# Kernel tuning notes

Measured on AMD Instinct MI355X. Metric: run time of the kernel, lower is better.

Reference implementation:

```python
import jax, jax.numpy as jnp
import numpy as np

DIM = 192
HEADS = 6
WS = 7
N = WS * WS
BW = 4096  # B_ = batch * num_windows
HIDDEN = int(DIM * 4.0)


def _relative_position_index():
    coords = np.stack(np.meshgrid(np.arange(WS), np.arange(WS), indexing='ij'))  # (2,ws,ws)
    cf = coords.reshape(2, -1)                      # (2, N)
    rel = cf[:, :, None] - cf[:, None, :]           # (2, N, N)
    rel = rel.transpose(1, 2, 0)                    # (N, N, 2)
    rel[:, :, 0] += WS - 1
    rel[:, :, 1] += WS - 1
    rel[:, :, 0] *= 2 * WS - 1
    return jnp.asarray(rel.sum(-1), dtype=jnp.int32)  # (N, N)


def setup_inputs() -> dict:
    key = jax.random.key(0)
    ks = jax.random.split(key, 8)
    s = 0.02
    return {
        'x': jax.random.normal(ks[0], (BW, N, DIM), dtype=jnp.float32),
        'ln1_g': jnp.ones((DIM,), jnp.float32),
        'ln1_b': jnp.zeros((DIM,), jnp.float32),
        'qkv_w': jax.random.normal(ks[1], (DIM, 3 * DIM), jnp.float32) * s,  # (in, out)
        'proj_w': jax.random.normal(ks[2], (DIM, DIM), jnp.float32) * s,
        'proj_b': jnp.zeros((DIM,), jnp.float32),
        'bias_table': jax.random.normal(ks[3], ((2 * WS - 1) ** 2, HEADS), jnp.float32) * s,
        'ln2_g': jnp.ones((DIM,), jnp.float32),
        'ln2_b': jnp.zeros((DIM,), jnp.float32),
        'fc1_w': jax.random.normal(ks[4], (DIM, HIDDEN), jnp.float32) * s,
        'fc1_b': jnp.zeros((HIDDEN,), jnp.float32),
        'fc2_w': jax.random.normal(ks[5], (HIDDEN, DIM), jnp.float32) * s,
        'fc2_b': jnp.zeros((DIM,), jnp.float32),
        'rel_index': _relative_position_index(),
    }


def _layer_norm(x, g, b, eps=1e-5):
    mu = jnp.mean(x, axis=-1, keepdims=True)
    var = jnp.var(x, axis=-1, keepdims=True)
    return (x - mu) * jax.lax.rsqrt(var + eps) * g + b


def _window_attention(x, qkv_w, proj_w, proj_b, bias_table, rel_index):
    B_, n, C = x.shape
    hd = C // HEADS
    scale = hd ** -0.5
    qkv = (x @ qkv_w).reshape(B_, n, 3, HEADS, hd)
    q, k, v = (qkv[:, :, i].transpose(0, 2, 1, 3) for i in range(3))  # (B_, h, n, hd)
    attn = jnp.einsum('bhnd,bhmd->bhnm', q * scale, k)
    bias = bias_table[rel_index.reshape(-1)].reshape(n, n, HEADS).transpose(2, 0, 1)
    attn = jax.nn.softmax(attn + bias[None], axis=-1)
    out = jnp.einsum('bhnm,bhmd->bhnd', attn, v).transpose(0, 2, 1, 3).reshape(B_, n, C)
    return out @ proj_w + proj_b


def reference(x, ln1_g, ln1_b, qkv_w, proj_w, proj_b, bias_table,
              ln2_g, ln2_b, fc1_w, fc1_b, fc2_w, fc2_b, rel_index):
    x = x + _window_attention(_layer_norm(x, ln1_g, ln1_b), qkv_w, proj_w, proj_b,
                              bias_table, rel_index)
    h = _layer_norm(x, ln2_g, ln2_b)
    h = jax.nn.gelu(h @ fc1_w + fc1_b, approximate=False) @ fc2_w + fc2_b
    return x + h
```

## Files before the change

### kernel.cpp

```cpp
#include <hip/hip_runtime.h>
#include <cmath>

#define TOK   49
#define WDIM  192
#define NHEADS 6
#define HID   768

typedef __bf16 bf16_t;
typedef bf16_t bf16x8 __attribute__((ext_vector_type(8)));
typedef float  f32x4  __attribute__((ext_vector_type(4)));

#define XLD  200
#define QKLD 72
#define VTLD 72
#define AOLD 72
#define PLD  40
#define HLD2 200

__device__ __forceinline__ f32x4 mfma16(bf16x8 a, bf16x8 b, f32x4 c) {
    return __builtin_amdgcn_mfma_f32_16x16x32_bf16(a, b, c, 0, 0, 0);
}

__device__ __forceinline__ float gelu_f(float v) {
    float u = 0.7978845608028654f * (v + 0.044715f * v * v * v);
    float e = __expf(2.f * u);
    float t = 1.f - 2.f / (e + 1.f);
    return 0.5f * v * (1.f + t);
}

__global__ void pack_w(const float* __restrict__ W, bf16_t* __restrict__ out,
                       int K, int N, int total) {
    int p = blockIdx.x * 256 + threadIdx.x;
    if (p >= total) return;
    int j    = p & 7;
    int lane = (p >> 3) & 63;
    int kbnt = p >> 9;
    int KB   = K >> 5;
    int kb   = kbnt % KB;
    int nt   = kbnt / KB;
    int n = nt * 16 + (lane & 15);
    int k = kb * 32 + (lane >> 4) * 8 + j;
    out[p] = (bf16_t)W[k * N + n];
}

__global__ void make_bias6(const float* __restrict__ table, const int* __restrict__ rel,
                           float* __restrict__ out) {
    int p = blockIdx.x * 256 + threadIdx.x;
    if (p >= NHEADS * TOK * TOK) return;
    int h  = p / (TOK * TOK);
    int mn = p % (TOK * TOK);
    out[p] = table[rel[mn] * NHEADS + h];
}

__global__ void __launch_bounds__(256, 2) attn_kernel(
    const float* __restrict__ x,
    const float* __restrict__ g1, const float* __restrict__ b1,
    const bf16_t* __restrict__ qkv_p, const bf16_t* __restrict__ proj_p,
    const float* __restrict__ proj_b, const float* __restrict__ bias6,
    float* __restrict__ out) {

    __shared__ bf16_t s_xln[64 * XLD];
    __shared__ bf16_t s_q[64 * QKLD];
    __shared__ bf16_t s_k[64 * QKLD];
    __shared__ bf16_t s_vT[64 * VTLD];
    __shared__ bf16_t s_ao[64 * AOLD];
    __shared__ bf16_t s_p[4][16 * PLD];

    const int t    = threadIdx.x;
    const int w    = t >> 6;
    const int lane = t & 63;
    const int l15  = lane & 15;
    const int quad = lane >> 4;
    const int widx = blockIdx.x;
    const float scale = 0.17677669529663687f;
    const f32x4 z = {0.f, 0.f, 0.f, 0.f};

    const float* xw = x + (size_t)widx * (TOK * WDIM);

    {
        int r = t >> 2, l4 = t & 3;
        if (r < TOK) {
            const float* row = xw + r * WDIM + l4 * 48;
            float s = 0.f, sq = 0.f;
            #pragma unroll
            for (int i = 0; i < 12; i++) {
                float4 f = ((const float4*)row)[i];
                s  += f.x + f.y + f.z + f.w;
                sq += f.x*f.x + f.y*f.y + f.z*f.z + f.w*f.w;
            }
            s  += __shfl_xor(s, 1);  s  += __shfl_xor(s, 2);
            sq += __shfl_xor(sq, 1); sq += __shfl_xor(sq, 2);
            float mean = s * (1.f / WDIM);
            float rstd = rsqrtf(sq * (1.f / WDIM) - mean * mean + 1e-5f);
            #pragma unroll
            for (int i = 0; i < 12; i++) {
                float4 f = ((const float4*)row)[i];
                int c = l4 * 48 + i * 4;
                s_xln[r * XLD + c + 0] = (bf16_t)((f.x - mean) * rstd * g1[c+0] + b1[c+0]);
                s_xln[r * XLD + c + 1] = (bf16_t)((f.y - mean) * rstd * g1[c+1] + b1[c+1]);
                s_xln[r * XLD + c + 2] = (bf16_t)((f.z - mean) * rstd * g1[c+2] + b1[c+2]);
                s_xln[r * XLD + c + 3] = (bf16_t)((f.w - mean) * rstd * g1[c+3] + b1[c+3]);
            }
        } else {
            #pragma unroll
            for (int i = 0; i < 48; i++)
                s_xln[r * XLD + l4 * 48 + i] = (bf16_t)0.f;
        }
    }
    __syncthreads();

    f32x4 pacc[4][3];
    #pragma unroll
    for (int rt = 0; rt < 4; rt++)
        #pragma unroll
        for (int j = 0; j < 3; j++) pacc[rt][j] = z;

    for (int pr = 0; pr < 3; pr++) {
        f32x4 qa[4][3];
        #pragma unroll
        for (int rt = 0; rt < 4; rt++)
            #pragma unroll
            for (int j = 0; j < 3; j++) qa[rt][j] = z;

        int ntg[3];
        #pragma unroll
        for (int j = 0; j < 3; j++) {
            int np = w * 3 + j;
            int g = np >> 2, hh = (np >> 1) & 1, d16 = np & 1;
            ntg[j] = g * 12 + (2 * pr + hh) * 2 + d16;
        }
        #pragma unroll
        for (int kb = 0; kb < 6; kb++) {
            bf16x8 a[4];
            #pragma unroll
            for (int rt = 0; rt < 4; rt++)
                a[rt] = *(const bf16x8*)&s_xln[(rt * 16 + l15) * XLD + kb * 32 + quad * 8];
            #pragma unroll
            for (int j = 0; j < 3; j++) {
                bf16x8 b = *(const bf16x8*)&qkv_p[(size_t)((ntg[j] * 6 + kb) * 64 + lane) * 8];
                #pragma unroll
                for (int rt = 0; rt < 4; rt++)
                    qa[rt][j] = mfma16(a[rt], b, qa[rt][j]);
            }
        }
        #pragma unroll
        for (int j = 0; j < 3; j++) {
            int np = w * 3 + j;
            int g = np >> 2;
            int pcol = ((np >> 1) & 1) * 32 + (np & 1) * 16 + l15;
            #pragma unroll
            for (int rt = 0; rt < 4; rt++)
                #pragma unroll
                for (int reg = 0; reg < 4; reg++) {
                    int row = rt * 16 + quad * 4 + reg;
                    bf16_t val = (bf16_t)qa[rt][j][reg];
                    if (g == 0)      s_q[row * QKLD + pcol] = val;
                    else if (g == 1) s_k[row * QKLD + pcol] = val;
                    else             s_vT[pcol * VTLD + row] = val;
                }
        }
        __syncthreads();

        #pragma unroll
        for (int hh = 0; hh < 2; hh++) {
            int h = 2 * pr + hh;
            bf16x8 aq = *(const bf16x8*)&s_q[(w * 16 + l15) * QKLD + hh * 32 + quad * 8];
            f32x4 sa[4];
            #pragma unroll
            for (int nt = 0; nt < 4; nt++) {
                bf16x8 bk = *(const bf16x8*)&s_k[(nt * 16 + l15) * QKLD + hh * 32 + quad * 8];
                sa[nt] = mfma16(aq, bk, z);
            }
            float p[4][4];
            const float* b6 = bias6 + h * (TOK * TOK);
            #pragma unroll
            for (int nt = 0; nt < 4; nt++) {
                int n  = nt * 16 + l15;
                int nc = (n < TOK) ? n : 0;
                #pragma unroll
                for (int reg = 0; reg < 4; reg++) {
                    int mm = w * 16 + quad * 4 + reg;
                    int mc = (mm < TOK) ? mm : 0;
                    float bias = b6[mc * TOK + nc];
                    p[nt][reg] = (n < TOK) ? (sa[nt][reg] * scale + bias) : -INFINITY;
                }
            }
            #pragma unroll
            for (int reg = 0; reg < 4; reg++) {
                float mx = fmaxf(fmaxf(p[0][reg], p[1][reg]), fmaxf(p[2][reg], p[3][reg]));
                mx = fmaxf(mx, __shfl_xor(mx, 1));
                mx = fmaxf(mx, __shfl_xor(mx, 2));
                mx = fmaxf(mx, __shfl_xor(mx, 4));
                mx = fmaxf(mx, __shfl_xor(mx, 8));
                float sum = 0.f;
                #pragma unroll
                for (int nt = 0; nt < 4; nt++) {
                    float e = __expf(p[nt][reg] - mx);
                    p[nt][reg] = e;
                    sum += e;
                }
                sum += __shfl_xor(sum, 1);
                sum += __shfl_xor(sum, 2);
                sum += __shfl_xor(sum, 4);
                sum += __shfl_xor(sum, 8);
                float rinv = 1.f / sum;
                #pragma unroll
                for (int nt = 0; nt < 4; nt++) p[nt][reg] *= rinv;
            }
            bf16_t* pw = s_p[w];
            f32x4 oa[2] = {z, z};
            #pragma unroll
            for (int hf = 0; hf < 2; hf++) {
                #pragma unroll
                for (int i = 0; i < 2; i++) {
                    int nt = hf * 2 + i;
                    #pragma unroll
                    for (int reg = 0; reg < 4; reg++)
                        pw[(quad * 4 + reg) * PLD + i * 16 + l15] = (bf16_t)p[nt][reg];
                }
                bf16x8 ap = *(const bf16x8*)&pw[l15 * PLD + quad * 8];
                #pragma unroll
                for (int dt = 0; dt < 2; dt++) {
                    bf16x8 bv = *(const bf16x8*)&s_vT[(hh * 32 + dt * 16 + l15) * VTLD + hf * 32 + quad * 8];
                    oa[dt] = mfma16(ap, bv, oa[dt]);
                }
            }
            #pragma unroll
            for (int dt = 0; dt < 2; dt++)
                #pragma unroll
                for (int reg = 0; reg < 4; reg++)
                    s_ao[(w * 16 + quad * 4 + reg) * AOLD + hh * 32 + dt * 16 + l15] = (bf16_t)oa[dt][reg];
        }
        __syncthreads();

        #pragma unroll
        for (int kbp = 0; kbp < 2; kbp++) {
            bf16x8 a[4];
            #pragma unroll
            for (int rt = 0; rt < 4; rt++)
                a[rt] = *(const bf16x8*)&s_ao[(rt * 16 + l15) * AOLD + kbp * 32 + quad * 8];
            #pragma unroll
            for (int j = 0; j < 3; j++) {
                int nt = w * 3 + j;
                bf16x8 b = *(const bf16x8*)&proj_p[(size_t)((nt * 6 + pr * 2 + kbp) * 64 + lane) * 8];
                #pragma unroll
                for (int rt = 0; rt < 4; rt++)
                    pacc[rt][j] = mfma16(a[rt], b, pacc[rt][j]);
            }
        }
    }

    float* ow = out + (size_t)widx * (TOK * WDIM);
    #pragma unroll
    for (int rt = 0; rt < 4; rt++)
        #pragma unroll
        for (int j = 0; j < 3; j++) {
            int col = (w * 3 + j) * 16 + l15;
            #pragma unroll
            for (int reg = 0; reg < 4; reg++) {
                int mm = rt * 16 + quad * 4 + reg;
                if (mm < TOK)
                    ow[mm * WDIM + col] = pacc[rt][j][reg] + proj_b[col] + xw[mm * WDIM + col];
            }
        }
}

__global__ void __launch_bounds__(256, 2) mlp_kernel(
    float* __restrict__ xio,
    const float* __restrict__ g2, const float* __restrict__ b2,
    const bf16_t* __restrict__ fc1_p, const float* __restrict__ fc1_b,
    const bf16_t* __restrict__ fc2_p, const float* __restrict__ fc2_b) {

    __shared__ bf16_t s_x[64 * XLD];
    __shared__ bf16_t s_h[64 * HLD2];

    const int t    = threadIdx.x;
    const int w    = t >> 6;
    const int lane = t & 63;
    const int l15  = lane & 15;
    const int quad = lane >> 4;
    const f32x4 z = {0.f, 0.f, 0.f, 0.f};
    float* xw = xio + (size_t)blockIdx.x * 64 * WDIM;

    {
        int r = t >> 2, l4 = t & 3;
        const float* row = xw + r * WDIM + l4 * 48;
        float s = 0.f, sq = 0.f;
        #pragma unroll
        for (int i = 0; i < 12; i++) {
            float4 f = ((const float4*)row)[i];
            s  += f.x + f.y + f.z + f.w;
            sq += f.x*f.x + f.y*f.y + f.z*f.z + f.w*f.w;
        }
        s  += __shfl_xor(s, 1);  s  += __shfl_xor(s, 2);
        sq += __shfl_xor(sq, 1); sq += __shfl_xor(sq, 2);
        float mean = s * (1.f / WDIM);
        float rstd = rsqrtf(sq * (1.f / WDIM) - mean * mean + 1e-5f);
        #pragma unroll
        for (int i = 0; i < 12; i++) {
            float4 f = ((const float4*)row)[i];
            int c = l4 * 48 + i * 4;
            s_x[r * XLD + c + 0] = (bf16_t)((f.x - mean) * rstd * g2[c+0] + b2[c+0]);
            s_x[r * XLD + c + 1] = (bf16_t)((f.y - mean) * rstd * g2[c+1] + b2[c+1]);
            s_x[r * XLD + c + 2] = (bf16_t)((f.z - mean) * rstd * g2[c+2] + b2[c+2]);
            s_x[r * XLD + c + 3] = (bf16_t)((f.w - mean) * rstd * g2[c+3] + b2[c+3]);
        }
    }
    __syncthreads();

    f32x4 fa[4][3];
    #pragma unroll
    for (int rt = 0; rt < 4; rt++)
        #pragma unroll
        for (int j = 0; j < 3; j++) fa[rt][j] = z;

    for (int ch = 0; ch < 4; ch++) {
        f32x4 ha[4][3];
        #pragma unroll
        for (int rt = 0; rt < 4; rt++)
            #pragma unroll
            for (int j = 0; j < 3; j++) ha[rt][j] = z;
        #pragma unroll
        for (int kb = 0; kb < 6; kb++) {
            bf16x8 a[4];
            #pragma unroll
            for (int rt = 0; rt < 4; rt++)
                a[rt] = *(const bf16x8*)&s_x[(rt * 16 + l15) * XLD + kb * 32 + quad * 8];
            #pragma unroll
            for (int j = 0; j < 3; j++) {
                int ntg = ch * 12 + w * 3 + j;
                bf16x8 b = *(const bf16x8*)&fc1_p[(size_t)((ntg * 6 + kb) * 64 + lane) * 8];
                #pragma unroll
                for (int rt = 0; rt < 4; rt++)
                    ha[rt][j] = mfma16(a[rt], b, ha[rt][j]);
            }
        }
        #pragma unroll
        for (int j = 0; j < 3; j++) {
            int colg = (ch * 12 + w * 3 + j) * 16 + l15;
            float fb = fc1_b[colg];
            int colc = (w * 3 + j) * 16 + l15;
            #pragma unroll
            for (int rt = 0; rt < 4; rt++)
                #pragma unroll
                for (int reg = 0; reg < 4; reg++) {
                    float v = ha[rt][j][reg] + fb;
                    s_h[(rt * 16 + quad * 4 + reg) * HLD2 + colc] = (bf16_t)gelu_f(v);
                }
        }
        __syncthreads();
        #pragma unroll
        for (int kc = 0; kc < 6; kc++) {
            bf16x8 a[4];
            #pragma unroll
            for (int rt = 0; rt < 4; rt++)
                a[rt] = *(const bf16x8*)&s_h[(rt * 16 + l15) * HLD2 + kc * 32 + quad * 8];
            int kbg = ch * 6 + kc;
            #pragma unroll
            for (int j = 0; j < 3; j++) {
                int nt = w * 3 + j;
                bf16x8 b = *(const bf16x8*)&fc2_p[(size_t)((nt * 24 + kbg) * 64 + lane) * 8];
                #pragma unroll
                for (int rt = 0; rt < 4; rt++)
                    fa[rt][j] = mfma16(a[rt], b, fa[rt][j]);
            }
        }
        __syncthreads();
    }

    #pragma unroll
    for (int rt = 0; rt < 4; rt++)
        #pragma unroll
        for (int j = 0; j < 3; j++) {
            int col = (w * 3 + j) * 16 + l15;
            #pragma unroll
            for (int reg = 0; reg < 4; reg++) {
                int r = rt * 16 + quad * 4 + reg;
                float* ptr = xw + r * WDIM + col;
                *ptr = fa[rt][j][reg] + fc2_b[col] + *ptr;
            }
        }
}

extern "C" void kernel_launch(void* const* d_in, const int* in_sizes, int n_in,
                              void* d_out, int out_size, void* d_ws, size_t ws_size,
                              hipStream_t stream) {
    const float* x      = (const float*)d_in[0];
    const float* ln1_g  = (const float*)d_in[1];
    const float* ln1_b  = (const float*)d_in[2];
    const float* qkv_w  = (const float*)d_in[3];
    const float* proj_w = (const float*)d_in[4];
    const float* proj_b = (const float*)d_in[5];
    const float* bias_t = (const float*)d_in[6];
    const float* ln2_g  = (const float*)d_in[7];
    const float* ln2_b  = (const float*)d_in[8];
    const float* fc1_w  = (const float*)d_in[9];
    const float* fc1_b  = (const float*)d_in[10];
    const float* fc2_w  = (const float*)d_in[11];
    const float* fc2_b  = (const float*)d_in[12];
    const int*   rel    = (const int*)d_in[13];
    float* out = (float*)d_out;

    char* ws = (char*)d_ws;
    bf16_t* qkv_p  = (bf16_t*)(ws);
    bf16_t* proj_p = (bf16_t*)(ws + 221184);
    bf16_t* fc1_p  = (bf16_t*)(ws + 294912);
    bf16_t* fc2_p  = (bf16_t*)(ws + 589824);
    float*  bias6  = (float*) (ws + 884736);

    pack_w<<<432, 256, 0, stream>>>(qkv_w,  qkv_p,  192, 576, 110592);
    pack_w<<<144, 256, 0, stream>>>(proj_w, proj_p, 192, 192,  36864);
    pack_w<<<576, 256, 0, stream>>>(fc1_w,  fc1_p,  192, 768, 147456);
    pack_w<<<576, 256, 0, stream>>>(fc2_w,  fc2_p,  768, 192, 147456);
    make_bias6<<<57, 256, 0, stream>>>(bias_t, rel, bias6);

    attn_kernel<<<4096, 256, 0, stream>>>(x, ln1_g, ln1_b, qkv_p, proj_p, proj_b, bias6, out);
    mlp_kernel<<<3136, 256, 0, stream>>>(out, ln2_g, ln2_b, fc1_p, fc1_b, fc2_p, fc2_b);
}
```

Before: 851.7 us.

## Restructure MLP into per-wave row tiles, merge prep kernels, cheaper GELU/softmax reciprocals

The MLP kernel is reorganized so each wave owns 16 rows and computes all fc2 output columns, with a private per-wave hidden buffer. This removes the block-wide __syncthreads between fc1 and fc2, shrinks shared memory, and raises the launch-bounds occupancy hint to 4 blocks. The price is that each wave now loads every weight fragment itself, instead of the block sharing them, so global and L2 weight traffic grows. The five weight-pack and bias setup launches are merged into one prep kernel. GELU is rewritten in the sigmoid form with a hardware reciprocal, and the softmax reciprocal uses rcpf.

```diff
diff --git a/kernel.cpp b/kernel.cpp
--- a/kernel.cpp
+++ b/kernel.cpp
@@ -15,23 +15,20 @@
 #define VTLD 72
 #define AOLD 72
 #define PLD  40
-#define HLD2 200
+#define HLD  104
 
 __device__ __forceinline__ f32x4 mfma16(bf16x8 a, bf16x8 b, f32x4 c) {
     return __builtin_amdgcn_mfma_f32_16x16x32_bf16(a, b, c, 0, 0, 0);
 }
 
 __device__ __forceinline__ float gelu_f(float v) {
-    float u = 0.7978845608028654f * (v + 0.044715f * v * v * v);
-    float e = __expf(2.f * u);
-    float t = 1.f - 2.f / (e + 1.f);
-    return 0.5f * v * (1.f + t);
-}
-
-__global__ void pack_w(const float* __restrict__ W, bf16_t* __restrict__ out,
-                       int K, int N, int total) {
-    int p = blockIdx.x * 256 + threadIdx.x;
-    if (p >= total) return;
+    float u2 = 1.5957691216057308f * v * __builtin_fmaf(0.044715f, v * v, 1.f);
+    float ee = __expf(-u2);
+    return v * __builtin_amdgcn_rcpf(1.f + ee);
+}
+
+__device__ __forceinline__ void pack_one(const float* __restrict__ W, bf16_t* __restrict__ out,
+                                         int K, int N, int p) {
     int j    = p & 7;
     int lane = (p >> 3) & 63;
     int kbnt = p >> 9;
@@ -43,13 +40,29 @@
     out[p] = (bf16_t)W[k * N + n];
 }
 
-__global__ void make_bias6(const float* __restrict__ table, const int* __restrict__ rel,
-                           float* __restrict__ out) {
-    int p = blockIdx.x * 256 + threadIdx.x;
-    if (p >= NHEADS * TOK * TOK) return;
-    int h  = p / (TOK * TOK);
-    int mn = p % (TOK * TOK);
-    out[p] = table[rel[mn] * NHEADS + h];
+__global__ void prep_kernel(const float* __restrict__ qkv_w, const float* __restrict__ proj_w,
+                            const float* __restrict__ fc1_w, const float* __restrict__ fc2_w,
+                            const float* __restrict__ table, const int* __restrict__ rel,
+                            bf16_t* __restrict__ qkv_p, bf16_t* __restrict__ proj_p,
+                            bf16_t* __restrict__ fc1_p, bf16_t* __restrict__ fc2_p,
+                            float* __restrict__ bias6) {
+    int b = blockIdx.x, t = threadIdx.x;
+    if (b < 432) {
+        pack_one(qkv_w, qkv_p, 192, 576, b * 256 + t);
+    } else if (b < 576) {
+        pack_one(proj_w, proj_p, 192, 192, (b - 432) * 256 + t);
+    } else if (b < 1152) {
+        pack_one(fc1_w, fc1_p, 192, 768, (b - 576) * 256 + t);
+    } else if (b < 1728) {
+        pack_one(fc2_w, fc2_p, 768, 192, (b - 1152) * 256 + t);
+    } else {
+        int p = (b - 1728) * 256 + t;
+        if (p < NHEADS * TOK * TOK) {
+            int h  = p / (TOK * TOK);
+            int mn = p % (TOK * TOK);
+            bias6[p] = table[rel[mn] * NHEADS + h];
+        }
+    }
 }
 
 __global__ void __launch_bounds__(256, 2) attn_kernel(
@@ -203,7 +216,7 @@
                 sum += __shfl_xor(sum, 2);
                 sum += __shfl_xor(sum, 4);
                 sum += __shfl_xor(sum, 8);
-                float rinv = 1.f / sum;
+                float rinv = __builtin_amdgcn_rcpf(sum);
                 #pragma unroll
                 for (int nt = 0; nt < 4; nt++) p[nt][reg] *= rinv;
             }
@@ -265,14 +278,14 @@
         }
 }
 
-__global__ void __launch_bounds__(256, 2) mlp_kernel(
+__global__ void __launch_bounds__(256, 4) mlp_kernel(
     float* __restrict__ xio,
     const float* __restrict__ g2, const float* __restrict__ b2,
     const bf16_t* __restrict__ fc1_p, const float* __restrict__ fc1_b,
     const bf16_t* __restrict__ fc2_p, const float* __restrict__ fc2_b) {
 
     __shared__ bf16_t s_x[64 * XLD];
-    __shared__ bf16_t s_h[64 * HLD2];
+    __shared__ bf16_t s_h[4][16 * HLD];
 
     const int t    = threadIdx.x;
     const int w    = t >> 6;
@@ -308,78 +321,57 @@
     }
     __syncthreads();
 
-    f32x4 fa[4][3];
+    const int r0 = w * 16;
+    bf16_t* hw = &s_h[w][0];
+
+    f32x4 fa[12];
     #pragma unroll
-    for (int rt = 0; rt < 4; rt++)
-        #pragma unroll
-        for (int j = 0; j < 3; j++) fa[rt][j] = z;
-
-    for (int ch = 0; ch < 4; ch++) {
-        f32x4 ha[4][3];
-        #pragma unroll
-        for (int rt = 0; rt < 4; rt++)
-            #pragma unroll
-            for (int j = 0; j < 3; j++) ha[rt][j] = z;
+    for (int j = 0; j < 12; j++) fa[j] = z;
+
+    for (int ch = 0; ch < 8; ch++) {
+        f32x4 ha[6];
+        #pragma unroll
+        for (int j = 0; j < 6; j++) ha[j] = z;
         #pragma unroll
         for (int kb = 0; kb < 6; kb++) {
-            bf16x8 a[4];
-            #pragma unroll
-            for (int rt = 0; rt < 4; rt++)
-                a[rt] = *(const bf16x8*)&s_x[(rt * 16 + l15) * XLD + kb * 32 + quad * 8];
-            #pragma unroll
-            for (int j = 0; j < 3; j++) {
-                int ntg = ch * 12 + w * 3 + j;
+            bf16x8 a = *(const bf16x8*)&s_x[(r0 + l15) * XLD + kb * 32 + quad * 8];
+            #pragma unroll
+            for (int j = 0; j < 6; j++) {
+                int ntg = ch * 6 + j;
                 bf16x8 b = *(const bf16x8*)&fc1_p[(size_t)((ntg * 6 + kb) * 64 + lane) * 8];
-                #pragma unroll
-                for (int rt = 0; rt < 4; rt++)
-                    ha[rt][j] = mfma16(a[rt], b, ha[rt][j]);
-            }
-        }
-        #pragma unroll
-        for (int j = 0; j < 3; j++) {
-            int colg = (ch * 12 + w * 3 + j) * 16 + l15;
-            float fb = fc1_b[colg];
-            int colc = (w * 3 + j) * 16 + l15;
-            #pragma unroll
-            for (int rt = 0; rt < 4; rt++)
-                #pragma unroll
-                for (int reg = 0; reg < 4; reg++) {
-                    float v = ha[rt][j][reg] + fb;
-                    s_h[(rt * 16 + quad * 4 + reg) * HLD2 + colc] = (bf16_t)gelu_f(v);
-                }
-        }
-        __syncthreads();
-        #pragma unroll
-        for (int kc = 0; kc < 6; kc++) {
-            bf16x8 a[4];
-            #pragma unroll
-            for (int rt = 0; rt < 4; rt++)
-                a[rt] = *(const bf16x8*)&s_h[(rt * 16 + l15) * HLD2 + kc * 32 + quad * 8];
-            int kbg = ch * 6 + kc;
-            #pragma unroll
-            for (int j = 0; j < 3; j++) {
-                int nt = w * 3 + j;
-                bf16x8 b = *(const bf16x8*)&fc2_p[(size_t)((nt * 24 + kbg) * 64 + lane) * 8];
-                #pragma unroll
-                for (int rt = 0; rt < 4; rt++)
-                    fa[rt][j] = mfma16(a[rt], b, fa[rt][j]);
-            }
-        }
-        __syncthreads();
+                ha[j] = mfma16(a, b, ha[j]);
+            }
+        }
+        #pragma unroll
+        for (int j = 0; j < 6; j++) {
+            float fb = fc1_b[(ch * 6 + j) * 16 + l15];
+            #pragma unroll
+            for (int reg = 0; reg < 4; reg++)
+                hw[(quad * 4 + reg) * HLD + j * 16 + l15] = (bf16_t)gelu_f(ha[j][reg] + fb);
+        }
+        #pragma unroll
+        for (int kc = 0; kc < 3; kc++) {
+            bf16x8 a2 = *(const bf16x8*)&hw[l15 * HLD + kc * 32 + quad * 8];
+            int kbg = ch * 3 + kc;
+            #pragma unroll
+            for (int j = 0; j < 12; j++) {
+                bf16x8 b = *(const bf16x8*)&fc2_p[(size_t)((j * 24 + kbg) * 64 + lane) * 8];
+                fa[j] = mfma16(a2, b, fa[j]);
+            }
+        }
     }
 
     #pragma unroll
-    for (int rt = 0; rt < 4; rt++)
-        #pragma unroll
-        for (int j = 0; j < 3; j++) {
-            int col = (w * 3 + j) * 16 + l15;
-            #pragma unroll
-            for (int reg = 0; reg < 4; reg++) {
-                int r = rt * 16 + quad * 4 + reg;
-                float* ptr = xw + r * WDIM + col;
-                *ptr = fa[rt][j][reg] + fc2_b[col] + *ptr;
-            }
-        }
+    for (int j = 0; j < 12; j++) {
+        int col = j * 16 + l15;
+        float fb = fc2_b[col];
+        #pragma unroll
+        for (int reg = 0; reg < 4; reg++) {
+            int r = r0 + quad * 4 + reg;
+            float* ptr = xw + r * WDIM + col;
+            *ptr = fa[j][reg] + fb + *ptr;
+        }
+    }
 }
 
 extern "C" void kernel_launch(void* const* d_in, const int* in_sizes, int n_in,
@@ -408,11 +400,8 @@
     bf16_t* fc2_p  = (bf16_t*)(ws + 589824);
     float*  bias6  = (float*) (ws + 884736);
 
-    pack_w<<<432, 256, 0, stream>>>(qkv_w,  qkv_p,  192, 576, 110592);
-    pack_w<<<144, 256, 0, stream>>>(proj_w, proj_p, 192, 192,  36864);
-    pack_w<<<576, 256, 0, stream>>>(fc1_w,  fc1_p,  192, 768, 147456);
-    pack_w<<<576, 256, 0, stream>>>(fc2_w,  fc2_p,  768, 192, 147456);
-    make_bias6<<<57, 256, 0, stream>>>(bias_t, rel, bias6);
+    prep_kernel<<<1785, 256, 0, stream>>>(qkv_w, proj_w, fc1_w, fc2_w, bias_t, rel,
+                                          qkv_p, proj_p, fc1_p, fc2_p, bias6);
 
     attn_kernel<<<4096, 256, 0, stream>>>(x, ln1_g, ln1_b, qkv_p, proj_p, proj_b, bias6, out);
     mlp_kernel<<<3136, 256, 0, stream>>>(out, ln2_g, ln2_b, fc1_p, fc1_b, fc2_p, fc2_b);
```

Result: slower. 1.179 ms (+38.4%).
